# Kernel tuning notes

Measured on AMD Instinct MI355X. Metric: run time of the kernel, lower is better.

Reference implementation:

```python
import jax, jax.numpy as jnp
import numpy as np

N_HEAD = 16


def setup_inputs() -> dict:
    key = jax.random.key(0)
    ks = jax.random.split(key, 6)
    B, T, H = 4, 2048, 1024
    inp = jax.random.normal(ks[0], (B, T, H), dtype=jnp.float32)
    # padding mask: valid prefix of random length in [T//2, T] per batch row
    lengths = jax.random.randint(ks[1], (B, 1), T // 2, T + 1)
    mask = jnp.arange(T)[None, :] < lengths  # (B, T) bool
    s = 0.02
    w_qkv = jax.random.normal(ks[2], (H, 3 * H), dtype=jnp.float32) * s
    b_qkv = jax.random.normal(ks[3], (3 * H,), dtype=jnp.float32) * s
    w_out = jax.random.normal(ks[4], (H, H), dtype=jnp.float32) * s
    b_out = jax.random.normal(ks[5], (H,), dtype=jnp.float32) * s
    return {"input": inp, "mask": mask, "w_qkv": w_qkv, "b_qkv": b_qkv,
            "w_out": w_out, "b_out": b_out}


def reference(input, mask, w_qkv, b_qkv, w_out, b_out):
    B, T, H = input.shape
    hd = H // N_HEAD
    qkv = input @ w_qkv + b_qkv                       # (B, T, 3H)
    q, k, v = jnp.split(qkv, 3, axis=-1)
    # (B, T, H) -> (B, nh, T, hd)
    q = q.reshape(B, T, N_HEAD, hd).transpose(0, 2, 1, 3)
    k = k.reshape(B, T, N_HEAD, hd).transpose(0, 2, 1, 3)
    v = v.reshape(B, T, N_HEAD, hd).transpose(0, 2, 1, 3)
    scores = jnp.einsum('bhqd,bhkd->bhqk', q, k) / jnp.sqrt(jnp.float32(hd))
    causal = jnp.tril(jnp.ones((T, T), dtype=bool))   # (T, T)
    full_mask = causal[None, None, :, :] & mask[:, None, None, :]  # (B,1,T,T) bcast over heads
    scores = jnp.where(full_mask, scores, -jnp.inf)
    attn = jax.nn.softmax(scores, axis=-1)            # (B, nh, T, T)
    o = jnp.einsum('bhqk,bhkd->bhqd', attn, v)        # (B, nh, T, hd)
    o = o.transpose(0, 2, 1, 3).reshape(B, T, H)
    return o @ w_out + b_out
```

## Files before the change

kernel.cpp:

```cpp
#include <hip/hip_runtime.h>
#include <math.h>

#define B_  4
#define T_  2048
#define H_  1024
#define NH  16
#define HD  64
#define H3  3072

typedef short bf16x8 __attribute__((ext_vector_type(8)));
typedef short bf16x4 __attribute__((ext_vector_type(4)));
typedef float f32x4  __attribute__((ext_vector_type(4)));
typedef float f32x16 __attribute__((ext_vector_type(16)));

#define SC2F 0.18033688011112042f

__device__ __forceinline__ unsigned short f2bf(float f) {
    union { float f; unsigned u; } v; v.f = f;
    unsigned u = v.u;
    unsigned r = (u + 0x7fffu + ((u >> 16) & 1u)) >> 16;
    return (unsigned short)r;
}

__device__ __forceinline__ void gload_lds16(const void* g, void* l) {
    __builtin_amdgcn_global_load_lds(
        (const __attribute__((address_space(1))) unsigned*)g,
        (__attribute__((address_space(3))) unsigned*)l, 16, 0, 0);
}

__device__ __forceinline__ f32x4 mfma_16x16x16_bf16(bf16x4 a, bf16x4 b, f32x4 c) {
#if __has_builtin(__builtin_amdgcn_mfma_f32_16x16x16_bf16)
    return __builtin_amdgcn_mfma_f32_16x16x16_bf16(a, b, c, 0, 0, 0);
#elif __has_builtin(__builtin_amdgcn_mfma_f32_16x16x16bf16_1k)
    return __builtin_amdgcn_mfma_f32_16x16x16bf16_1k(a, b, c, 0, 0, 0);
#else
    f32x4 d;
    asm volatile("v_mfma_f32_16x16x16_bf16 %0, %1, %2, %3"
                 : "=v"(d) : "v"(a), "v"(b), "v"(c));
    return d;
#endif
}

__global__ void lengths_kernel(const void* mask, int* lengths) {
    int b = blockIdx.x;
    int t = threadIdx.x;
    const unsigned* mu = (const unsigned*)mask;
    bool is_byte = (mu[0] == 0x01010101u);
    int cnt = 0;
    if (is_byte) {
        const unsigned char* m8 = (const unsigned char*)mask;
        for (int i = t; i < T_; i += 256) cnt += (m8[b * T_ + i] != 0);
    } else {
        const unsigned* m32 = (const unsigned*)mask;
        for (int i = t; i < T_; i += 256) cnt += (m32[b * T_ + i] != 0);
    }
    __shared__ int red[256];
    red[t] = cnt;
    __syncthreads();
    for (int s = 128; s > 0; s >>= 1) {
        if (t < s) red[t] += red[t + s];
        __syncthreads();
    }
    if (t == 0) lengths[b] = red[0];
}

__global__ void convert_bf16_kernel(const float* __restrict__ x,
                                    unsigned short* __restrict__ y, int n) {
    int i = (blockIdx.x * 256 + threadIdx.x) * 4;
    if (i < n) {
        float4 v = *(const float4*)(x + i);
        ushort4 o;
        o.x = f2bf(v.x); o.y = f2bf(v.y); o.z = f2bf(v.z); o.w = f2bf(v.w);
        *(ushort4*)(y + i) = o;
    }
}

__global__ void transpose2_kernel(const float* __restrict__ Wqkv,
                                  unsigned short* __restrict__ WqkvT,
                                  const float* __restrict__ Wout,
                                  unsigned short* __restrict__ WoutT) {
    __shared__ unsigned short tile[32][33];
    const int K = H_;
    const float* in;
    unsigned short* out;
    int N, nb;
    if (blockIdx.x < 96) { in = Wqkv; out = WqkvT; N = H3; nb = blockIdx.x * 32; }
    else                 { in = Wout; out = WoutT; N = H_; nb = (blockIdx.x - 96) * 32; }
    int kb = blockIdx.y * 32;
    int tx = threadIdx.x, ty = threadIdx.y;
    for (int i = 0; i < 32; i += 8)
        tile[ty + i][tx] = f2bf(in[(long)(kb + ty + i) * N + nb + tx]);
    __syncthreads();
    for (int i = 0; i < 32; i += 8)
        out[(long)(nb + ty + i) * K + kb + tx] = tile[tx][ty + i];
}

template <int TN, bool BF16_OUT, bool KSCALE, bool VSPLIT>
__global__ __launch_bounds__(256) void gemm_kernel(
    const unsigned short* __restrict__ A,
    const unsigned short* __restrict__ Bt,
    const float* __restrict__ bias,
    void* __restrict__ C,
    unsigned short* __restrict__ Vt,
    int M, int N, int K)
{
    __shared__ unsigned short Asm[128][64];
    __shared__ unsigned short Bsm[TN][64];

    int tn = blockIdx.x * TN, tm = blockIdx.y * 128;
    int tid = threadIdx.x;
    int wid = tid >> 6, lane = tid & 63;
    int l31 = lane & 31, lh = lane >> 5;
    int wm = (wid & 1) * 64, wn = (wid >> 1) * (TN / 2);

    int rl = lane >> 3;
    int g8 = ((lane & 7) ^ rl) * 8;
    const unsigned short* aP = A  + (long)(tm + wid * 32 + rl) * K + g8;
    const unsigned short* bP = Bt + (long)(tn + wid * (TN / 4) + rl) * K + g8;
    int rk = l31 & 7;

    f32x16 acc[2][TN / 64] = {};

    for (int k0 = 0; k0 < K; k0 += 64) {
        __syncthreads();
#pragma unroll
        for (int t = 0; t < 4; t++)
            gload_lds16(aP + (long)(t * 8) * K + k0, &Asm[wid * 32 + t * 8][0]);
#pragma unroll
        for (int t = 0; t < TN / 32; t++)
            gload_lds16(bP + (long)(t * 8) * K + k0, &Bsm[wid * (TN / 4) + t * 8][0]);
        __syncthreads();

#pragma unroll
        for (int ks = 0; ks < 4; ks++) {
            int pc = ((ks * 2 + lh) ^ rk) * 8;
            bf16x8 af[2], bv[TN / 64];
            af[0] = *(const bf16x8*)(&Asm[wm + l31][pc]);
            af[1] = *(const bf16x8*)(&Asm[wm + 32 + l31][pc]);
#pragma unroll
            for (int j = 0; j < TN / 64; j++)
                bv[j] = *(const bf16x8*)(&Bsm[wn + j * 32 + l31][pc]);
#pragma unroll
            for (int i = 0; i < 2; i++)
#pragma unroll
                for (int j = 0; j < TN / 64; j++)
                    acc[i][j] = __builtin_amdgcn_mfma_f32_32x32x16_bf16(
                        af[i], bv[j], acc[i][j], 0, 0, 0);
        }
    }

    if (VSPLIT && tn >= 2 * H_) {
#pragma unroll
        for (int i = 0; i < 2; i++)
#pragma unroll
            for (int j = 0; j < TN / 64; j++) {
                int col = tn + wn + j * 32 + l31;
                float bs = bias[col];
                int feat = col - 2 * H_;
#pragma unroll
                for (int rg = 0; rg < 4; rg++) {
                    int tok0 = tm + wm + i * 32 + rg * 8 + lh * 4;
                    int bb = tok0 >> 11;
                    unsigned d0 = (unsigned)f2bf(acc[i][j][rg * 4 + 0] + bs) |
                                  ((unsigned)f2bf(acc[i][j][rg * 4 + 1] + bs) << 16);
                    unsigned d1 = (unsigned)f2bf(acc[i][j][rg * 4 + 2] + bs) |
                                  ((unsigned)f2bf(acc[i][j][rg * 4 + 3] + bs) << 16);
                    unsigned short* dst = Vt + ((long)(bb * 1024 + feat)) * T_ + (tok0 & (T_ - 1));
                    *(uint2*)dst = make_uint2(d0, d1);
                }
            }
        return;
    }

#pragma unroll
    for (int i = 0; i < 2; i++)
#pragma unroll
        for (int j = 0; j < TN / 64; j++) {
            int col = tn + wn + j * 32 + l31;
            float bs = bias[col];
            bool ks_ = KSCALE && (col >= H_) && (col < 2 * H_);
#pragma unroll
            for (int r = 0; r < 16; r++) {
                int row = tm + wm + i * 32 + (r & 3) + 8 * (r >> 2) + 4 * lh;
                float v = acc[i][j][r] + bs;
                if (ks_) v *= SC2F;
                if (BF16_OUT)
                    ((unsigned short*)C)[(long)row * N + col] = f2bf(v);
                else
                    ((float*)C)[(long)row * N + col] = v;
            }
        }
}

__global__ __launch_bounds__(256) void attn_kernel(
    const unsigned short* __restrict__ QKV,
    const unsigned short* __restrict__ Vt,
    const int* __restrict__ lengths,
    unsigned short* __restrict__ O)
{
    int idx = blockIdx.x;
    int bh = idx & 63;
    int qt = 15 - (idx >> 6);
    int b = bh >> 4, h = bh & 15;
    int len = lengths[b];
    int q0 = qt * 128;

    int tid = threadIdx.x;
    int wid = tid >> 6, lane = tid & 63, quad = lane >> 4, lr = lane & 15;
    int quad4 = quad * 4;

    __shared__ __align__(16) unsigned short SH[16384];
    unsigned short (*Kd)[64][64] = (unsigned short (*)[64][64])(&SH[0]);
    unsigned short (*Vd)[64][64] = (unsigned short (*)[64][64])(&SH[8192]);

    const long qkv_base = (long)b * T_ * H3;

    bf16x8 qf[2][2];
#pragma unroll
    for (int nq = 0; nq < 2; nq++)
#pragma unroll
        for (int ks = 0; ks < 2; ks++)
            qf[nq][ks] = *(const bf16x8*)(QKV + qkv_base +
                (long)(q0 + wid * 32 + nq * 16 + lr) * H3 + h * HD + ks * 32 + quad * 8);

    int rl = lane >> 3;
    int g8 = ((lane & 7) ^ rl) * 8;
    const unsigned short* kB = QKV + qkv_base + (long)(wid * 16 + rl) * H3 + H_ + h * HD + g8;
    const unsigned short* vB = Vt + (long)(bh * 64 + wid * 16 + rl) * T_ + g8;

    f32x4 lacc[2] = {};
    f32x4 Oacc[4][2] = {};

    int kmax = min(q0 + 127, len - 1);
    int n_kt = (kmax >> 6) + 1;
    int q_wave_lo = q0 + wid * 32;
    int qwl_u = __builtin_amdgcn_readfirstlane(q_wave_lo);
    int q_wave_hi = qwl_u + 31;
    int bnd_[2] = { min(q_wave_lo + lr, len - 1),
                    min(q_wave_lo + 16 + lr, len - 1) };
    int rk = lr & 7;

    const short oneb = (short)0x3F80;
    bf16x4 vones = { oneb, oneb, oneb, oneb };

#pragma unroll
    for (int t = 0; t < 2; t++) {
        gload_lds16(kB + (long)(t * 8) * H3, &Kd[0][wid * 16 + t * 8][0]);
        gload_lds16(vB + (long)(t * 8) * T_, &Vd[0][wid * 16 + t * 8][0]);
    }

    for (int kt = 0; kt < n_kt; kt++) {
        int cur = kt & 1;
        __syncthreads();

        if (kt + 1 < n_kt) {
            long koff = (long)((kt + 1) * 64) * H3;
            int voff = (kt + 1) * 64;
#pragma unroll
            for (int t = 0; t < 2; t++) {
                gload_lds16(kB + koff + (long)(t * 8) * H3, &Kd[cur ^ 1][wid * 16 + t * 8][0]);
                gload_lds16(vB + (long)(t * 8) * T_ + voff, &Vd[cur ^ 1][wid * 16 + t * 8][0]);
            }
        }

        int k_lo = kt * 64;
        if (k_lo > q_wave_hi || k_lo >= len) continue;

        int mt_hi = min(q_wave_hi, len - 1);
        int nmt = min(4, ((mt_hi - k_lo) >> 4) + 1);
        nmt = __builtin_amdgcn_readfirstlane(nmt);

        f32x4 Sacc[4][2] = {};
        __builtin_amdgcn_s_setprio(1);
#pragma unroll
        for (int mt = 0; mt < 4; mt++) {
            if (mt >= nmt) continue;
#pragma unroll
            for (int ks = 0; ks < 2; ks++) {
                bf16x8 kf = *(const bf16x8*)(&Kd[cur][mt * 16 + lr][((ks * 4 + quad) ^ rk) * 8]);
                Sacc[mt][0] = __builtin_amdgcn_mfma_f32_16x16x32_bf16(kf, qf[0][ks], Sacc[mt][0], 0, 0, 0);
                Sacc[mt][1] = __builtin_amdgcn_mfma_f32_16x16x32_bf16(kf, qf[1][ks], Sacc[mt][1], 0, 0, 0);
            }
        }
        __builtin_amdgcn_s_setprio(0);

        unsigned pkk[4][2][2];
#pragma unroll
        for (int mt = 0; mt < 4; mt++) {
            if (mt >= nmt) continue;
            int kb0 = k_lo + mt * 16;
            int kbl = kb0 + quad4;
#pragma unroll
            for (int nq = 0; nq < 2; nq++) {
                float p[4];
                if (kb0 + 15 <= qwl_u + nq * 16 && kb0 + 15 < len) {
#pragma unroll
                    for (int r = 0; r < 4; r++)
                        p[r] = __builtin_amdgcn_exp2f(Sacc[mt][nq][r]);
                } else {
                    int dlt = bnd_[nq] - kbl;
#pragma unroll
                    for (int r = 0; r < 4; r++) {
                        float s = (r <= dlt) ? Sacc[mt][nq][r] : -INFINITY;
                        p[r] = __builtin_amdgcn_exp2f(s);
                    }
                }
                pkk[mt][nq][0] = __builtin_amdgcn_perm(__float_as_uint(p[1]), __float_as_uint(p[0]), 0x07060302);
                pkk[mt][nq][1] = __builtin_amdgcn_perm(__float_as_uint(p[3]), __float_as_uint(p[2]), 0x07060302);
            }
        }

        __builtin_amdgcn_s_setprio(1);
#pragma unroll
        for (int mt = 0; mt < 4; mt++) {
            if (mt >= nmt) continue;
            union { unsigned u[2]; bf16x4 v; } bu[2];
            bu[0].u[0] = pkk[mt][0][0]; bu[0].u[1] = pkk[mt][0][1];
            bu[1].u[0] = pkk[mt][1][0]; bu[1].u[1] = pkk[mt][1][1];
            lacc[0] = mfma_16x16x16_bf16(vones, bu[0].v, lacc[0]);
            lacc[1] = mfma_16x16x16_bf16(vones, bu[1].v, lacc[1]);
#pragma unroll
            for (int md = 0; md < 4; md++) {
                bf16x4 vf = *(const bf16x4*)(&Vd[cur][md * 16 + lr]
                    [((mt * 2 + (quad >> 1)) ^ rk) * 8 + (quad & 1) * 4]);
                Oacc[md][0] = mfma_16x16x16_bf16(vf, bu[0].v, Oacc[md][0]);
                Oacc[md][1] = mfma_16x16x16_bf16(vf, bu[1].v, Oacc[md][1]);
            }
        }
        __builtin_amdgcn_s_setprio(0);
    }

    __syncthreads();
    {
        unsigned short (*Es)[68] = (unsigned short (*)[68])(&SH[0]);
        float inv[2] = { 1.f / lacc[0][0], 1.f / lacc[1][0] };
#pragma unroll
        for (int nq = 0; nq < 2; nq++)
#pragma unroll
            for (int md = 0; md < 4; md++)
#pragma unroll
                for (int rp = 0; rp < 2; rp++) {
                    float e0 = Oacc[md][nq][rp * 2]     * inv[nq];
                    float e1 = Oacc[md][nq][rp * 2 + 1] * inv[nq];
                    unsigned w = __builtin_amdgcn_perm(__float_as_uint(e1), __float_as_uint(e0), 0x07060302);
                    *(unsigned*)(&Es[wid * 32 + nq * 16 + lr][md * 16 + quad * 4 + rp * 2]) = w;
                }
        __asm__ volatile("s_waitcnt lgkmcnt(0)" ::: "memory");
        int row = lane >> 1, cb = (lane & 1) * 32;
        long tok = (long)b * T_ + q0 + wid * 32 + row;
#pragma unroll
        for (int i = 0; i < 4; i++) {
            float4 v = *(const float4*)(&Es[wid * 32 + row][cb + i * 8]);
            *(float4*)(&O[tok * H_ + h * HD + cb + i * 8]) = v;
        }
    }
}

extern "C" void kernel_launch(void* const* d_in, const int* in_sizes, int n_in,
                              void* d_out, int out_size, void* d_ws, size_t ws_size,
                              hipStream_t stream) {
    const float* X    = (const float*)d_in[0];
    const void*  mask = d_in[1];
    const float* Wqkv = (const float*)d_in[2];
    const float* bqkv = (const float*)d_in[3];
    const float* Wout = (const float*)d_in[4];
    const float* bout = (const float*)d_in[5];

    char* ws = (char*)d_ws;
    int* lengths          = (int*)ws;
    unsigned short* WqkvT = (unsigned short*)(ws + 256);
    unsigned short* WoutT = WqkvT + (long)H3 * H_;
    unsigned short* QKV   = WoutT + (long)H_ * H_;
    unsigned short* Xbf   = QKV + (long)B_ * T_ * H3;
    unsigned short* Vt    = Xbf + (long)B_ * T_ * H_;
    unsigned short* Obf   = Xbf;

    const int M = B_ * T_;

    lengths_kernel<<<B_, 256, 0, stream>>>(mask, lengths);
    convert_bf16_kernel<<<(M * H_ / 4 + 255) / 256, 256, 0, stream>>>(X, Xbf, M * H_);
    transpose2_kernel<<<dim3(128, H_ / 32), dim3(32, 8), 0, stream>>>(Wqkv, WqkvT, Wout, WoutT);
    gemm_kernel<128, true, true, true><<<dim3(H3 / 128, M / 128), 256, 0, stream>>>(
        Xbf, WqkvT, bqkv, QKV, Vt, M, H3, H_);
    attn_kernel<<<B_ * NH * (T_ / 128), 256, 0, stream>>>(QKV, Vt, lengths, Obf);
    gemm_kernel<64, false, false, false><<<dim3(H_ / 64, M / 128), 256, 0, stream>>>(
        Obf, WoutT, bout, d_out, nullptr, M, H_, H_);
}
```

Baseline: 277.8 us.

## Double-buffer GEMM LDS tiles and remap block IDs across XCDs

The GEMM kernel now keeps two LDS buffers for the A and B tiles. It prefetches the next K-slice into the spare buffer while MFMAs run on the current one, which drops one barrier per iteration and hides global-load latency. Block indices are also remapped so that consecutive tiles go to the same XCD group, aiming for better L2 reuse. The cost is double the LDS per block, which may lower occupancy, and the remap assumes the total block count is divisible by 8.

```diff
diff --git a/kernel.cpp b/kernel.cpp
--- a/kernel.cpp
+++ b/kernel.cpp
@@ -104,10 +104,16 @@
     unsigned short* __restrict__ Vt,
     int M, int N, int K)
 {
-    __shared__ unsigned short Asm[128][64];
-    __shared__ unsigned short Bsm[TN][64];
-
-    int tn = blockIdx.x * TN, tm = blockIdx.y * 128;
+    __shared__ unsigned short Asm[2][128][64];
+    __shared__ unsigned short Bsm[2][TN][64];
+
+    int nbx = gridDim.x;
+    int bid = blockIdx.y * nbx + blockIdx.x;
+    int cpx = (nbx * gridDim.y) >> 3;
+    int lin = (bid & 7) * cpx + (bid >> 3);
+    int bx = lin % nbx, by = lin / nbx;
+
+    int tn = bx * TN, tm = by * 128;
     int tid = threadIdx.x;
     int wid = tid >> 6, lane = tid & 63;
     int l31 = lane & 31, lh = lane >> 5;
@@ -121,25 +127,35 @@
 
     f32x16 acc[2][TN / 64] = {};
 
+#pragma unroll
+    for (int t = 0; t < 4; t++)
+        gload_lds16(aP + (long)(t * 8) * K, &Asm[0][wid * 32 + t * 8][0]);
+#pragma unroll
+    for (int t = 0; t < TN / 32; t++)
+        gload_lds16(bP + (long)(t * 8) * K, &Bsm[0][wid * (TN / 4) + t * 8][0]);
+
+    int cur = 0;
     for (int k0 = 0; k0 < K; k0 += 64) {
         __syncthreads();
-#pragma unroll
-        for (int t = 0; t < 4; t++)
-            gload_lds16(aP + (long)(t * 8) * K + k0, &Asm[wid * 32 + t * 8][0]);
-#pragma unroll
-        for (int t = 0; t < TN / 32; t++)
-            gload_lds16(bP + (long)(t * 8) * K + k0, &Bsm[wid * (TN / 4) + t * 8][0]);
-        __syncthreads();
+
+        if (k0 + 64 < K) {
+#pragma unroll
+            for (int t = 0; t < 4; t++)
+                gload_lds16(aP + (long)(t * 8) * K + k0 + 64, &Asm[cur ^ 1][wid * 32 + t * 8][0]);
+#pragma unroll
+            for (int t = 0; t < TN / 32; t++)
+                gload_lds16(bP + (long)(t * 8) * K + k0 + 64, &Bsm[cur ^ 1][wid * (TN / 4) + t * 8][0]);
+        }
 
 #pragma unroll
         for (int ks = 0; ks < 4; ks++) {
             int pc = ((ks * 2 + lh) ^ rk) * 8;
             bf16x8 af[2], bv[TN / 64];
-            af[0] = *(const bf16x8*)(&Asm[wm + l31][pc]);
-            af[1] = *(const bf16x8*)(&Asm[wm + 32 + l31][pc]);
+            af[0] = *(const bf16x8*)(&Asm[cur][wm + l31][pc]);
+            af[1] = *(const bf16x8*)(&Asm[cur][wm + 32 + l31][pc]);
 #pragma unroll
             for (int j = 0; j < TN / 64; j++)
-                bv[j] = *(const bf16x8*)(&Bsm[wn + j * 32 + l31][pc]);
+                bv[j] = *(const bf16x8*)(&Bsm[cur][wn + j * 32 + l31][pc]);
 #pragma unroll
             for (int i = 0; i < 2; i++)
 #pragma unroll
@@ -147,6 +163,7 @@
                     acc[i][j] = __builtin_amdgcn_mfma_f32_32x32x16_bf16(
                         af[i], bv[j], acc[i][j], 0, 0, 0);
         }
+        cur ^= 1;
     }
 
     if (VSPLIT && tn >= 2 * H_) {
```

After: 269.9 us. 1.03x faster.
